# Kernel optimization log

Measured on AMD Instinct MI355X. Metric: run time of the kernel, lower is better.

Reference implementation:

```python
import jax, jax.numpy as jnp
import numpy as np

D_MODEL = 512
NUM_HEADS = 6
MIN_DIM = 8


def _compute_integer_dims(head_dims_float):
    # Faithful numpy port of torch _compute_integer_dims (runs under no_grad in torch,
    # so it is a constant w.r.t. autodiff; computed on concrete values here).
    hdf = np.asarray(head_dims_float)
    hdi = np.floor(hdf).astype(np.int64)
    diff = int(D_MODEL - hdi.sum())
    res = hdf - np.floor(hdf)
    if diff > 0:
        idx = np.argsort(-res)[:diff]  # topk largest residuals
        hdi[idx] += 1
    elif diff < 0:
        idx = np.argsort(res)[:(-diff)]  # topk of -residuals = smallest residuals
        hdi[idx] -= 1
    return hdi


def setup_inputs() -> dict:
    key = jax.random.key(0)
    k1, k2, k3, k4, k5, k6 = jax.random.split(key, 6)
    B, T = 4, 2048
    s = 1.0 / np.sqrt(D_MODEL).astype(np.float32)
    return {
        "query": jax.random.normal(k1, (B, T, D_MODEL), dtype=jnp.float32),
        "head_weight_logits": jax.random.normal(k2, (NUM_HEADS,), dtype=jnp.float32),
        "w_qkv": jax.random.normal(k3, (D_MODEL, 3 * D_MODEL), dtype=jnp.float32) * s,
        "b_qkv": jax.random.normal(k4, (3 * D_MODEL,), dtype=jnp.float32) * 0.01,
        "w_out": jax.random.normal(k5, (D_MODEL, D_MODEL), dtype=jnp.float32) * s,
        "b_out": jax.random.normal(k6, (D_MODEL,), dtype=jnp.float32) * 0.01,
    }


def reference(query, head_weight_logits, w_qkv, b_qkv, w_out, b_out):
    head_ratios = jax.nn.softmax(head_weight_logits, axis=0)
    head_dims_float = MIN_DIM + head_ratios * (D_MODEL - MIN_DIM * NUM_HEADS)
    hdi = _compute_integer_dims(jax.lax.stop_gradient(head_dims_float))  # concrete ints

    qkv = query @ w_qkv + b_qkv                      # [B,T,3*D]
    q_all, k_all, v_all = jnp.split(qkv, 3, axis=-1)  # each [B,T,D]

    outs = []
    start = 0
    for i in range(NUM_HEADS):  # small fixed loop; heads have distinct ragged widths
        dim = int(hdi[i])
        q = q_all[..., start:start + dim]
        k = k_all[..., start:start + dim]
        v = v_all[..., start:start + dim]
        start += dim
        scores = jnp.einsum('btd,bsd->bts', q, k) / (float(dim) ** 0.5)  # [B,T,T]
        attn = jax.nn.softmax(scores, axis=-1)
        outs.append(jnp.einsum('bts,bsd->btd', attn, v))

    output = jnp.concatenate(outs, axis=-1) @ w_out + b_out  # [B,T,D]

    hdi_f = jnp.asarray(hdi, dtype=head_dims_float.dtype)
    float_loss = (head_dims_float.sum() - D_MODEL) ** 2 \
        + jnp.mean(jax.nn.relu(MIN_DIM - head_dims_float))
    int_loss = jnp.mean((head_dims_float - hdi_f) ** 2)
    return output, float_loss + 0.5 * int_loss
```

## Files before the change

kernel.cpp:

```cpp
#include <hip/hip_runtime.h>
#include <hip/hip_bf16.h>
#include <cstdint>

typedef __attribute__((ext_vector_type(8))) __bf16 bf16x8;
typedef __attribute__((ext_vector_type(8))) unsigned short u16x8;
typedef __attribute__((ext_vector_type(4))) float f32x4;

#define QKSTRIDE 640
#define QKROW 1280
#define VTPAD 528

static __device__ __forceinline__ unsigned short f2bf(float f) {
  __hip_bfloat16 h = __float2bfloat16(f);
  return *reinterpret_cast<unsigned short*>(&h);
}
static __device__ __forceinline__ float bf2f(unsigned short u) {
  union { unsigned v; float f; } c; c.v = ((unsigned)u) << 16; return c.f;
}
static __device__ __forceinline__ unsigned pack2bf(float a, float b) {
  return (unsigned)f2bf(a) | ((unsigned)f2bf(b) << 16);
}

static __device__ __forceinline__ void gload_lds16(const void* g, void* lds) {
  __builtin_amdgcn_global_load_lds(
      (const __attribute__((address_space(1))) unsigned int*)g,
      (__attribute__((address_space(3))) unsigned int*)lds, 16, 0, 0);
}

__global__ void prep_kernel(const float* __restrict__ logits, int* __restrict__ hdr,
                            int* __restrict__ cmap, int* __restrict__ sched,
                            float* __restrict__ loss_out) {
  __shared__ int sh_starts[8], sh_astarts[8];
  __shared__ int sh_ax[24], sh_apos[24], sh_ah[24], sh_ab[24];
  const int tid = threadIdx.x;
  if (blockIdx.x != 0) return;

  if (tid == 0) {
    float l[6]; float mx = -1e30f;
    for (int i = 0; i < 6; ++i) { l[i] = logits[i]; mx = fmaxf(mx, l[i]); }
    float e[6]; float s = 0.f;
    for (int i = 0; i < 6; ++i) { e[i] = expf(l[i] - mx); s += e[i]; }
    float hdf[6]; float sumh = 0.f;
    for (int i = 0; i < 6; ++i) { hdf[i] = 8.0f + (e[i] / s) * 464.0f; sumh += hdf[i]; }
    int hdi[6]; float res[6]; int isum = 0;
    for (int i = 0; i < 6; ++i) {
      float fl = floorf(hdf[i]);
      hdi[i] = (int)fl; res[i] = hdf[i] - fl; isum += hdi[i];
    }
    int diff = 512 - isum;
    bool used[6] = {false, false, false, false, false, false};
    if (diff > 0) {
      for (int t = 0; t < diff; ++t) {
        int best = -1; float bv = -1e30f;
        for (int i = 0; i < 6; ++i) if (!used[i] && res[i] > bv) { bv = res[i]; best = i; }
        used[best] = true; hdi[best] += 1;
      }
    } else if (diff < 0) {
      for (int t = 0; t < -diff; ++t) {
        int best = -1; float bv = 1e30f;
        for (int i = 0; i < 6; ++i) if (!used[i] && res[i] < bv) { bv = res[i]; best = i; }
        used[best] = true; hdi[best] -= 1;
      }
    }
    { int st = 0, ast = 0;
      for (int i = 0; i < 6; ++i) {
        sh_starts[i] = st; sh_astarts[i] = ast;
        hdr[i] = hdi[i]; hdr[8 + i] = st; hdr[16 + i] = ast;
        st += hdi[i]; ast += (hdi[i] + 7) & ~7;
      }
      sh_starts[6] = st; sh_starts[7] = st;
    }
    int csth[6];
    for (int i = 0; i < 6; ++i) {
      int ncl = (hdi[i] + 31) / 32;
      int ntl = (hdi[i] + 15) / 16;
      csth[i] = 4 * ncl + 2 * ntl + 8;
    }
    int ord[6] = {0, 1, 2, 3, 4, 5};
    for (int a = 0; a < 6; ++a)
      for (int c = a + 1; c < 6; ++c)
        if (csth[ord[c]] > csth[ord[a]]) { int t = ord[a]; ord[a] = ord[c]; ord[c] = t; }
    int binload[8], bincnt[8];
    for (int x = 0; x < 8; ++x) { binload[x] = 0; bincnt[x] = 0; }
    int na = 0;
    for (int a = 0; a < 6; ++a) {
      const int hh = ord[a];
      for (int bb = 0; bb < 4; ++bb) {
        int best = -1;
        for (int x = 0; x < 8; ++x)
          if (bincnt[x] + 64 <= 192 && (best < 0 || binload[x] < binload[best])) best = x;
        if (best < 0) best = 0;
        sh_ax[na] = best; sh_apos[na] = bincnt[best];
        sh_ah[na] = hh; sh_ab[na] = bb; ++na;
        bincnt[best] += 64;
        binload[best] += csth[hh];
      }
    }
    float dv = sumh - 512.0f;
    float floss = dv * dv;
    float rsum = 0.f;
    for (int i = 0; i < 6; ++i) rsum += fmaxf(8.0f - hdf[i], 0.0f);
    floss += rsum / 6.0f;
    float il = 0.f;
    for (int i = 0; i < 6; ++i) { float dd = hdf[i] - (float)hdi[i]; il += dd * dd; }
    il /= 6.0f;
    loss_out[0] = floss + 0.5f * il;
  }
  __syncthreads();

  for (int col = tid; col < 512; col += 64) {
    int hh = 5;
    for (int i = 0; i < 5; ++i) if (col < sh_starts[i + 1]) { hh = i; break; }
    int qc = sh_astarts[hh] + (col - sh_starts[hh]);
    cmap[col] = qc;
    cmap[512 + col] = QKSTRIDE + qc;
    cmap[1024 + col] = 4096 + col;
    cmap[1536 + col] = hh;
  }
  for (int e = tid; e < 1536; e += 64) sched[e] = -1;
  __syncthreads();
  for (int e = tid; e < 24 * 64; e += 64) {
    const int a = e >> 6, qi = e & 63;
    sched[sh_ax[a] + 8 * (sh_apos[a] + qi)] = sh_ah[a] | (sh_ab[a] << 4) | (qi << 8);
  }
}

__global__ void conv_bf16_kernel(const float* __restrict__ x, unsigned short* __restrict__ y, int n4) {
  int i = blockIdx.x * blockDim.x + threadIdx.x;
  if (i >= n4) return;
  float4 v = reinterpret_cast<const float4*>(x)[i];
  union { unsigned short u[4]; uint2 q; } o;
  o.u[0] = f2bf(v.x); o.u[1] = f2bf(v.y); o.u[2] = f2bf(v.z); o.u[3] = f2bf(v.w);
  reinterpret_cast<uint2*>(y)[i] = o.q;
}

__global__ void convWT2_kernel(const float* __restrict__ Wqkv, const float* __restrict__ Wout,
                               unsigned short* __restrict__ wqkvT, unsigned short* __restrict__ woutT) {
  __shared__ float tile[64][65];
  const int mz = blockIdx.z;
  if (mz && blockIdx.y >= 8) return;
  const int N = mz ? 512 : 1536;
  const float* W = mz ? Wout : Wqkv;
  unsigned short* WT = mz ? woutT : wqkvT;
  const int k0 = blockIdx.x * 64, n0 = blockIdx.y * 64;
  const int t = threadIdx.x;
  {
    const int c = (t & 15) * 4;
#pragma unroll
    for (int rp = 0; rp < 4; ++rp) {
      const int r = rp * 16 + (t >> 4);
      float4 v = *reinterpret_cast<const float4*>(&W[(size_t)(k0 + r) * N + n0 + c]);
      tile[r][c] = v.x; tile[r][c + 1] = v.y; tile[r][c + 2] = v.z; tile[r][c + 3] = v.w;
    }
  }
  __syncthreads();
  {
    const int n = t >> 2, kc = (t & 3) * 16;
    unsigned short outv[16];
#pragma unroll
    for (int j = 0; j < 16; ++j) outv[j] = f2bf(tile[kc + j][n]);
    unsigned short* dst = &WT[(size_t)(n0 + n) * 512 + k0 + kc];
    *reinterpret_cast<u16x8*>(dst) = *reinterpret_cast<u16x8*>(&outv[0]);
    *reinterpret_cast<u16x8*>(dst + 8) = *reinterpret_cast<u16x8*>(&outv[8]);
  }
}

template<int MODE>
__global__ __launch_bounds__(256, 2) void gemm_bt(
    const unsigned short* __restrict__ A,
    const unsigned short* __restrict__ Bt,
    const float* __restrict__ bias,
    float* __restrict__ Cf,
    unsigned short* __restrict__ qkpad,
    unsigned short* __restrict__ VtOut,
    const int* __restrict__ cmap,
    int N, int K)
{
  __shared__ unsigned short As[128 * 32];
  __shared__ unsigned short Bs[128 * 32];
  const int tid = threadIdx.x;
  const int wave = tid >> 6, lane = tid & 63;
  const int lrow = lane & 15, lgrp = lane >> 4;
  const int wm = wave >> 1, wn = wave & 1;
  const int brow = blockIdx.y * 128;
  const int bcol = blockIdx.x * 128;

  f32x4 acc[4][4];
#pragma unroll
  for (int m = 0; m < 4; ++m)
#pragma unroll
    for (int n = 0; n < 4; ++n) acc[m][n] = (f32x4){0.f, 0.f, 0.f, 0.f};

  const int sig0 = wave * 128 + lane;
  for (int kb = 0; kb < K; kb += 32) {
    __syncthreads();
#pragma unroll
    for (int it = 0; it < 2; ++it) {
      const int sigma = sig0 + it * 64;
      const int r = sigma >> 2, sp = sigma & 3;
      const int sl = sp ^ ((r >> 1) & 3);
      gload_lds16(&A[(size_t)(brow + r) * K + kb + sl * 8], &As[sigma * 8]);
    }
#pragma unroll
    for (int it = 0; it < 2; ++it) {
      const int sigma = sig0 + it * 64;
      const int r = sigma >> 2, sp = sigma & 3;
      const int sl = sp ^ ((r >> 1) & 3);
      gload_lds16(&Bt[(size_t)(bcol + r) * K + kb + sl * 8], &Bs[sigma * 8]);
    }
    __syncthreads();
    const int sub = (lgrp ^ ((lrow >> 1) & 3)) * 8;
    bf16x8 aF[4], bF[4];
#pragma unroll
    for (int m = 0; m < 4; ++m)
      aF[m] = *reinterpret_cast<const bf16x8*>(&As[(wm * 64 + m * 16 + lrow) * 32 + sub]);
#pragma unroll
    for (int n = 0; n < 4; ++n)
      bF[n] = *reinterpret_cast<const bf16x8*>(&Bs[(wn * 64 + n * 16 + lrow) * 32 + sub]);
#pragma unroll
    for (int m = 0; m < 4; ++m)
#pragma unroll
      for (int n = 0; n < 4; ++n)
        acc[m][n] = __builtin_amdgcn_mfma_f32_16x16x32_bf16(aF[m], bF[n], acc[m][n], 0, 0, 0);
  }

#pragma unroll
  for (int n = 0; n < 4; ++n) {
    const int col = bcol + wn * 64 + n * 16 + lrow;
    const float bv = bias[col];
    int mc = 0;
    if (MODE == 1) mc = cmap[col];
#pragma unroll
    for (int m = 0; m < 4; ++m) {
      if (MODE == 0) {
#pragma unroll
        for (int r = 0; r < 4; ++r) {
          const int row = brow + wm * 64 + m * 16 + lgrp * 4 + r;
          Cf[(size_t)row * N + col] = acc[m][n][r] + bv;
        }
      } else if (mc < 4096) {
#pragma unroll
        for (int r = 0; r < 4; ++r) {
          const int row = brow + wm * 64 + m * 16 + lgrp * 4 + r;
          qkpad[(size_t)row * QKROW + mc] = f2bf(acc[m][n][r] + bv);
        }
      } else {
        const int t0g = brow + wm * 64 + m * 16 + lgrp * 4;
        const int b = t0g >> 11, t0 = t0g & 2047;
        uint2 w;
        w.x = pack2bf(acc[m][n][0] + bv, acc[m][n][1] + bv);
        w.y = pack2bf(acc[m][n][2] + bv, acc[m][n][3] + bv);
        *reinterpret_cast<uint2*>(&VtOut[(size_t)(b * VTPAD + (mc - 4096)) * 2048 + t0]) = w;
      }
    }
  }
}

template<int NC>
static __device__ __forceinline__ void attn_body(
    const unsigned short* __restrict__ qkpad,
    const unsigned short* __restrict__ Vt,
    unsigned short* __restrict__ Op,
    float2* __restrict__ mlArr,
    int b, int q0, int d, int start, int astart, int kh, int mlBase,
    unsigned char* KsB, unsigned int* PlW,
    int wave, int lane)
{
  constexpr int S = (4 * NC + 7) & ~7;
  constexpr int NT2 = 2 * NC;
  constexpr int KI = S / 8;
  constexpr int KTILE = 32 * S * 16;
  const int ntiles = (d + 15) >> 4;
  const int lrow = lane & 15, lgrp = lane >> 4;
  const float scale = 1.0f / sqrtf((float)d);

  bf16x8 qf[NC];
  {
    const unsigned short* qp = qkpad + (size_t)(b * 2048 + q0 + lrow) * QKROW + astart + lgrp * 8;
#pragma unroll
    for (int dc = 0; dc < NC; ++dc) {
      bf16x8 v = *reinterpret_cast<const bf16x8*>(qp + dc * 32);
#pragma unroll
      for (int j = 0; j < 8; ++j)
        if (dc * 32 + lgrp * 8 + j >= d) v[j] = (__bf16)0.0f;
      qf[dc] = v;
    }
  }

  const unsigned short* kPtr[KI];
  int kDstB[KI];
#pragma unroll
  for (int j = 0; j < KI; ++j) {
    const int g = (wave * KI + j) * 64 + lane;
    const int r = g / S, pp = g - r * S;
    const int sp = pp ^ (r & 7);
    kPtr[j] = qkpad + (size_t)(b * 2048 + kh * 1024 + r) * QKROW + QKSTRIDE + astart + sp * 8;
    kDstB[j] = g * 16;
  }

  const unsigned short* vRow = Vt + (size_t)(b * VTPAD + start + lrow) * 2048 + kh * 1024 + lgrp * 8;

  f32x4 acc[NT2];
#pragma unroll
  for (int t = 0; t < NT2; ++t) acc[t] = (f32x4){0.f, 0.f, 0.f, 0.f};
  float m_run = -1e30f, l_run = 0.f;

#pragma unroll
  for (int j = 0; j < KI; ++j) gload_lds16(kPtr[j], KsB + kDstB[j]);
#pragma unroll
  for (int j = 0; j < KI; ++j) kPtr[j] += 32 * QKROW;
  __syncthreads();

  for (int i = 0; i < 32; ++i) {
    const int kt = i << 5;
    const int cur = i & 1;
    if (i < 31) {
      unsigned char* kd = KsB + (cur ^ 1) * KTILE;
#pragma unroll
      for (int j = 0; j < KI; ++j) gload_lds16(kPtr[j], kd + kDstB[j]);
#pragma unroll
      for (int j = 0; j < KI; ++j) kPtr[j] += 32 * QKROW;
    }

    f32x4 s4[2];
    s4[0] = (f32x4){0.f, 0.f, 0.f, 0.f};
    s4[1] = (f32x4){0.f, 0.f, 0.f, 0.f};
    const unsigned char* kB = KsB + cur * KTILE;
    const int swz = lrow & 7;
    __builtin_amdgcn_s_setprio(1);
#pragma unroll
    for (int dc = 0; dc < NC; ++dc) {
#pragma unroll
      for (int t = 0; t < 2; ++t) {
        const bf16x8 kf = *reinterpret_cast<const bf16x8*>(
            kB + (t * 16 + lrow) * (S * 16) + (((dc * 4 + lgrp) ^ swz) * 16));
        s4[t] = __builtin_amdgcn_mfma_f32_16x16x32_bf16(kf, qf[dc], s4[t], 0, 0, 0);
      }
    }
    __builtin_amdgcn_s_setprio(0);

    float ps[8];
#pragma unroll
    for (int t = 0; t < 2; ++t)
#pragma unroll
      for (int r = 0; r < 4; ++r) ps[t * 4 + r] = s4[t][r] * scale;
    float pm = ps[0];
#pragma unroll
    for (int z = 1; z < 8; ++z) pm = fmaxf(pm, ps[z]);
    pm = fmaxf(pm, __shfl_xor(pm, 16));
    pm = fmaxf(pm, __shfl_xor(pm, 32));
    if (__any(pm > m_run + 8.0f)) {
      const float mn = fmaxf(m_run, pm);
      const float alpha = __expf(m_run - mn);
      m_run = mn; l_run *= alpha;
      float al4[4];
#pragma unroll
      for (int r = 0; r < 4; ++r) al4[r] = __shfl(alpha, lgrp * 4 + r);
#pragma unroll
      for (int t = 0; t < NT2; ++t) {
        if (t < ntiles) {
#pragma unroll
          for (int r = 0; r < 4; ++r) acc[t][r] *= al4[r];
        }
      }
    }
    float sum = 0.f;
#pragma unroll
    for (int z = 0; z < 8; ++z) { ps[z] = __expf(ps[z] - m_run); sum += ps[z]; }
    sum += __shfl_xor(sum, 16);
    sum += __shfl_xor(sum, 32);
    l_run += sum;

#pragma unroll
    for (int t = 0; t < 2; ++t) {
      uint2 w;
      w.x = pack2bf(ps[t * 4 + 0], ps[t * 4 + 1]);
      w.y = pack2bf(ps[t * 4 + 2], ps[t * 4 + 3]);
      *reinterpret_cast<uint2*>(PlW + lrow * 20 + 8 * t + 2 * lgrp) = w;
    }
    asm volatile("s_waitcnt lgkmcnt(0)" ::: "memory");
    __builtin_amdgcn_sched_barrier(0);
    const bf16x8 pa = *reinterpret_cast<const bf16x8*>(PlW + lrow * 20 + 4 * lgrp);

#pragma unroll
    for (int t0 = 0; t0 < NT2; t0 += 8) {
      bf16x8 vf[8];
#pragma unroll
      for (int j = 0; j < 8; ++j) {
        const int t = t0 + j;
        if (t < NT2 && t < ntiles)
          vf[j] = *reinterpret_cast<const bf16x8*>(vRow + (size_t)t * 32768 + kt);
      }
      __builtin_amdgcn_s_setprio(1);
#pragma unroll
      for (int j = 0; j < 8; ++j) {
        const int t = t0 + j;
        if (t < NT2 && t < ntiles)
          acc[t] = __builtin_amdgcn_mfma_f32_16x16x32_bf16(pa, vf[j], acc[t], 0, 0, 0);
      }
      __builtin_amdgcn_s_setprio(0);
    }
    __syncthreads();
  }

  float invl[4];
#pragma unroll
  for (int r = 0; r < 4; ++r) invl[r] = 1.0f / __shfl(l_run, lgrp * 4 + r);
#pragma unroll
  for (int t = 0; t < NT2; ++t) {
    if (t < ntiles) {
      const int col = t * 16 + lrow;
      if (col < d) {
#pragma unroll
        for (int r = 0; r < 4; ++r) {
          Op[(size_t)(b * 2048 + q0 + lgrp * 4 + r) * 512 + start + col] =
              f2bf(acc[t][r] * invl[r]);
        }
      }
    }
  }
  if (lgrp == 0) mlArr[mlBase + lrow] = make_float2(m_run, l_run);
}

__global__ __launch_bounds__(256, 3) void attn_fused(
    const unsigned short* __restrict__ qkpad,
    const unsigned short* __restrict__ Vt,
    unsigned short* __restrict__ O0,
    unsigned short* __restrict__ O1,
    float2* __restrict__ mlArr,
    const int* __restrict__ hdr,
    const int* __restrict__ sched)
{
  __shared__ __align__(16) unsigned char KsB[32768];
  __shared__ unsigned int Pl[4][16 * 20];

  const int sv = sched[blockIdx.x];
  if (sv < 0) return;
  const int h = sv & 15, b = (sv >> 4) & 15;
  const int qi = (sv >> 8) & 63;
  const int qb = qi & 31, kh = qi >> 5;
  const int d = hdr[h];
  const int nc = (d + 31) >> 5;
  if (nc > 8) return;
  const int start = hdr[8 + h];
  const int astart = hdr[16 + h];
  const int wave = threadIdx.x >> 6, lane = threadIdx.x & 63;
  const int q0 = qb * 64 + wave * 16;
  unsigned short* Op = kh ? O1 : O0;
  const int mlBase = (kh * 24 + h * 4 + b) * 2048 + q0;

  unsigned int* PlW = &Pl[wave][0];
  switch (nc) {
    case 1: attn_body<1>(qkpad, Vt, Op, mlArr, b, q0, d, start, astart, kh, mlBase, KsB, PlW, wave, lane); break;
    case 2: attn_body<2>(qkpad, Vt, Op, mlArr, b, q0, d, start, astart, kh, mlBase, KsB, PlW, wave, lane); break;
    case 3: attn_body<3>(qkpad, Vt, Op, mlArr, b, q0, d, start, astart, kh, mlBase, KsB, PlW, wave, lane); break;
    case 4: attn_body<4>(qkpad, Vt, Op, mlArr, b, q0, d, start, astart, kh, mlBase, KsB, PlW, wave, lane); break;
    case 5: attn_body<5>(qkpad, Vt, Op, mlArr, b, q0, d, start, astart, kh, mlBase, KsB, PlW, wave, lane); break;
    case 6: attn_body<6>(qkpad, Vt, Op, mlArr, b, q0, d, start, astart, kh, mlBase, KsB, PlW, wave, lane); break;
    case 7: attn_body<7>(qkpad, Vt, Op, mlArr, b, q0, d, start, astart, kh, mlBase, KsB, PlW, wave, lane); break;
    case 8: attn_body<8>(qkpad, Vt, Op, mlArr, b, q0, d, start, astart, kh, mlBase, KsB, PlW, wave, lane); break;
    default: break;
  }
}

__global__ __launch_bounds__(256) void merge_kernel(
    const unsigned short* __restrict__ O0,
    const unsigned short* __restrict__ O1,
    const float2* __restrict__ mlArr,
    unsigned short* __restrict__ attnC,
    const int* __restrict__ hdr)
{
  const int sh = blockIdx.y;
  const int h = sh >> 2, b = sh & 3;
  const int d = hdr[h];
  if (((d + 31) >> 5) > 8) return;
  const int start = hdr[8 + h];
  const int q = blockIdx.x * 32 + (threadIdx.x >> 3);
  const int cg = threadIdx.x & 7;
  const float2 A = mlArr[(h * 4 + b) * 2048 + q];
  const float2 B = mlArr[(24 + h * 4 + b) * 2048 + q];
  const float M = fmaxf(A.x, B.x);
  const float a1 = __expf(A.x - M) * A.y;
  const float a2 = __expf(B.x - M) * B.y;
  const float inv = 1.0f / (a1 + a2);
  const float r1 = a1 * inv, r2 = a2 * inv;
  const size_t base = (size_t)(b * 2048 + q) * 512 + start;
  for (int c = cg; c < d; c += 8)
    attnC[base + c] = f2bf(r1 * bf2f(O0[base + c]) + r2 * bf2f(O1[base + c]));
}

template<int NCLO, int NCHI>
__global__ __launch_bounds__(256, 2) void attn_kernel(
    const unsigned short* __restrict__ qkpad,
    const unsigned short* __restrict__ Vt,
    unsigned short* __restrict__ attnC,
    const int* __restrict__ hdr)
{
  const int h = blockIdx.y, b = blockIdx.z;
  const int d = hdr[h];
  const int nc = (d + 31) >> 5;
  if (nc <= NCLO || nc > NCHI) return;
  const int start = hdr[8 + h];
  const int astart = hdr[16 + h];
  const int wave = threadIdx.x >> 6;
  const int lane = threadIdx.x & 63;
  const int lrow = lane & 15, lgrp = lane >> 4;
  const int q0 = blockIdx.x * 64 + wave * 16;
  const int ntiles = (d + 15) >> 4;
  const float scale = 1.0f / sqrtf((float)d);

  __shared__ unsigned short Pl[2][4][16 * 32];

  bf16x8 qf[NCHI];
  {
    const size_t qbase = (size_t)(b * 2048 + q0 + lrow) * QKROW + astart;
#pragma unroll
    for (int dc = 0; dc < NCHI; ++dc) {
      if (dc < nc) {
        bf16x8 v = *reinterpret_cast<const bf16x8*>(&qkpad[qbase + dc * 32 + lgrp * 8]);
#pragma unroll
        for (int j = 0; j < 8; ++j)
          if (dc * 32 + lgrp * 8 + j >= d) v[j] = (__bf16)0.0f;
        qf[dc] = v;
      }
    }
  }

  f32x4 acc[2 * NCHI];
#pragma unroll
  for (int t = 0; t < 2 * NCHI; ++t) acc[t] = (f32x4){0.f, 0.f, 0.f, 0.f};
  float m_run[4] = {-1e30f, -1e30f, -1e30f, -1e30f};
  float l_run[4] = {0.f, 0.f, 0.f, 0.f};

  for (int kt = 0; kt < 2048; kt += 32) {
    f32x4 s0 = {0.f, 0.f, 0.f, 0.f}, s1 = {0.f, 0.f, 0.f, 0.f};
    const size_t kb0 = (size_t)(b * 2048 + kt + lrow) * QKROW + QKSTRIDE + astart;
    const size_t kb1 = kb0 + (size_t)16 * QKROW;
#pragma unroll
    for (int dc = 0; dc < NCHI; ++dc) {
      if (dc < nc) {
        bf16x8 k0 = *reinterpret_cast<const bf16x8*>(&qkpad[kb0 + dc * 32 + lgrp * 8]);
        bf16x8 k1 = *reinterpret_cast<const bf16x8*>(&qkpad[kb1 + dc * 32 + lgrp * 8]);
        s0 = __builtin_amdgcn_mfma_f32_16x16x32_bf16(qf[dc], k0, s0, 0, 0, 0);
        s1 = __builtin_amdgcn_mfma_f32_16x16x32_bf16(qf[dc], k1, s1, 0, 0, 0);
      }
    }
    float p0[4], p1[4], pmax[4];
#pragma unroll
    for (int r = 0; r < 4; ++r) {
      p0[r] = s0[r] * scale; p1[r] = s1[r] * scale;
      float mx = fmaxf(p0[r], p1[r]);
#pragma unroll
      for (int off = 1; off < 16; off <<= 1) mx = fmaxf(mx, __shfl_xor(mx, off));
      pmax[r] = mx;
    }
    bool need = false;
#pragma unroll
    for (int r = 0; r < 4; ++r) need = need || (pmax[r] > m_run[r] + 8.0f);
    if (__any(need)) {
#pragma unroll
      for (int r = 0; r < 4; ++r) {
        float mn = fmaxf(m_run[r], pmax[r]);
        float al = __expf(m_run[r] - mn);
        m_run[r] = mn; l_run[r] *= al;
#pragma unroll
        for (int t = 0; t < 2 * NCHI; ++t)
          if (t < ntiles) acc[t][r] *= al;
      }
    }
#pragma unroll
    for (int r = 0; r < 4; ++r) {
      p0[r] = __expf(p0[r] - m_run[r]);
      p1[r] = __expf(p1[r] - m_run[r]);
      float sm = p0[r] + p1[r];
#pragma unroll
      for (int off = 1; off < 16; off <<= 1) sm += __shfl_xor(sm, off);
      l_run[r] += sm;
    }
    const int pb = (kt >> 5) & 1;
    unsigned short* P = &Pl[pb][wave][0];
#pragma unroll
    for (int r = 0; r < 4; ++r) {
      P[(lgrp * 4 + r) * 32 + lrow] = f2bf(p0[r]);
      P[(lgrp * 4 + r) * 32 + 16 + lrow] = f2bf(p1[r]);
    }
    asm volatile("s_waitcnt lgkmcnt(0)" ::: "memory");
    bf16x8 pf = *reinterpret_cast<const bf16x8*>(&P[lrow * 32 + lgrp * 8]);
    const size_t vbase = (size_t)(b * VTPAD + start) * 2048 + kt + lgrp * 8;
#pragma unroll
    for (int t = 0; t < 2 * NCHI; ++t) {
      if (t < ntiles) {
        bf16x8 vf = *reinterpret_cast<const bf16x8*>(&Vt[vbase + (size_t)(t * 16 + lrow) * 2048]);
        acc[t] = __builtin_amdgcn_mfma_f32_16x16x32_bf16(pf, vf, acc[t], 0, 0, 0);
      }
    }
  }

  float inv[4];
#pragma unroll
  for (int r = 0; r < 4; ++r) inv[r] = 1.0f / l_run[r];
#pragma unroll
  for (int t = 0; t < 2 * NCHI; ++t) {
    if (t < ntiles) {
      int col = t * 16 + lrow;
      if (col < d) {
#pragma unroll
        for (int r = 0; r < 4; ++r) {
          attnC[(size_t)(b * 2048 + q0 + lgrp * 4 + r) * 512 + start + col] =
              f2bf(acc[t][r] * inv[r]);
        }
      }
    }
  }
}

extern "C" void kernel_launch(void* const* d_in, const int* in_sizes, int n_in,
                              void* d_out, int out_size, void* d_ws, size_t ws_size,
                              hipStream_t stream) {
  const float* query  = (const float*)d_in[0];
  const float* logits = (const float*)d_in[1];
  const float* w_qkv  = (const float*)d_in[2];
  const float* b_qkv  = (const float*)d_in[3];
  const float* w_out  = (const float*)d_in[4];
  const float* b_out  = (const float*)d_in[5];
  float* out = (float*)d_out;

  char* p = (char*)d_ws;
  size_t off = 0;
  auto alloc = [&](size_t bytes) {
    void* r = p + off; off += (bytes + 255) & ~(size_t)255; return r;
  };
  int* hdr              = (int*)alloc(1024);
  int* cmap             = (int*)alloc(2048 * 4);
  int* sched            = (int*)alloc(1536 * 4);
  unsigned short* qbf   = (unsigned short*)alloc((size_t)8192 * 512 * 2);
  unsigned short* wqkvT = (unsigned short*)alloc((size_t)1536 * 512 * 2);
  unsigned short* woutT = (unsigned short*)alloc((size_t)512 * 512 * 2);
  unsigned short* qkpad = (unsigned short*)alloc((size_t)8192 * QKROW * 2 + 4096);
  unsigned short* vbuf  = (unsigned short*)alloc((size_t)8192 * 512 * 2);
  unsigned short* Vt    = (unsigned short*)alloc((size_t)4 * VTPAD * 2048 * 2 + 4096);
  unsigned short* attnC = (unsigned short*)alloc((size_t)8192 * 512 * 2);
  float2* mlArr         = (float2*)alloc((size_t)2 * 24 * 2048 * 8);
  (void)ws_size; (void)in_sizes; (void)n_in; (void)out_size;

  prep_kernel<<<1, 64, 0, stream>>>(logits, hdr, cmap, sched, out + 4194304);
  conv_bf16_kernel<<<4096, 256, 0, stream>>>(query, qbf, 8192 * 512 / 4);
  convWT2_kernel<<<dim3(8, 24, 2), 256, 0, stream>>>(w_qkv, w_out, wqkvT, woutT);
  gemm_bt<1><<<dim3(12, 64), 256, 0, stream>>>(qbf, wqkvT, b_qkv, nullptr, qkpad, Vt, cmap, 1536, 512);
  attn_fused<<<dim3(1536, 1, 1), 256, 0, stream>>>(qkpad, Vt, qbf, vbuf, mlArr, hdr, sched);
  attn_kernel<8, 15><<<dim3(32, 6, 4), 256, 0, stream>>>(qkpad, Vt, attnC, hdr);
  merge_kernel<<<dim3(64, 24), 256, 0, stream>>>(qbf, vbuf, mlArr, attnC, hdr);
  gemm_bt<0><<<dim3(4, 64), 256, 0, stream>>>(attnC, woutT, b_out, out, nullptr, nullptr, nullptr, 512, 512);
}
```

Before: 284.2 us.

## Split wide-head attention blocks across output-dim halves and rebalance schedule

For heads with more than four 32-column chunks, each block now covers 32 queries instead of 64, and pairs of waves split the output head dimension in halves. Each wave holds at most 8 accumulator tiles, so register pressure drops and the launch bound goes from 3 to 4 blocks per CU. The scheduler assigns 128 slots to wide heads with a larger per-bin capacity, and the grid grows to 2560 blocks. The trade-off is that QK^T and softmax are computed twice, once per wave in each pair, which adds redundant compute and K loads.

```diff
diff --git a/kernel.cpp b/kernel.cpp
--- a/kernel.cpp
+++ b/kernel.cpp
@@ -31,7 +31,7 @@
                             int* __restrict__ cmap, int* __restrict__ sched,
                             float* __restrict__ loss_out) {
   __shared__ int sh_starts[8], sh_astarts[8];
-  __shared__ int sh_ax[24], sh_apos[24], sh_ah[24], sh_ab[24];
+  __shared__ int sh_ax[24], sh_apos[24], sh_ah[24], sh_ab[24], sh_nb[24];
   const int tid = threadIdx.x;
   if (blockIdx.x != 0) return;
 
@@ -70,11 +70,12 @@
       }
       sh_starts[6] = st; sh_starts[7] = st;
     }
-    int csth[6];
+    int csth[6], nbh6[6];
     for (int i = 0; i < 6; ++i) {
       int ncl = (hdi[i] + 31) / 32;
       int ntl = (hdi[i] + 15) / 16;
       csth[i] = 4 * ncl + 2 * ntl + 8;
+      nbh6[i] = (ncl <= 4) ? 64 : 128;
     }
     int ord[6] = {0, 1, 2, 3, 4, 5};
     for (int a = 0; a < 6; ++a)
@@ -85,14 +86,15 @@
     int na = 0;
     for (int a = 0; a < 6; ++a) {
       const int hh = ord[a];
+      const int nb = nbh6[hh];
       for (int bb = 0; bb < 4; ++bb) {
         int best = -1;
         for (int x = 0; x < 8; ++x)
-          if (bincnt[x] + 64 <= 192 && (best < 0 || binload[x] < binload[best])) best = x;
+          if (bincnt[x] + nb <= 320 && (best < 0 || binload[x] < binload[best])) best = x;
         if (best < 0) best = 0;
         sh_ax[na] = best; sh_apos[na] = bincnt[best];
-        sh_ah[na] = hh; sh_ab[na] = bb; ++na;
-        bincnt[best] += 64;
+        sh_ah[na] = hh; sh_ab[na] = bb; sh_nb[na] = nb; ++na;
+        bincnt[best] += nb;
         binload[best] += csth[hh];
       }
     }
@@ -117,11 +119,12 @@
     cmap[1024 + col] = 4096 + col;
     cmap[1536 + col] = hh;
   }
-  for (int e = tid; e < 1536; e += 64) sched[e] = -1;
+  for (int e = tid; e < 2560; e += 64) sched[e] = -1;
   __syncthreads();
-  for (int e = tid; e < 24 * 64; e += 64) {
-    const int a = e >> 6, qi = e & 63;
-    sched[sh_ax[a] + 8 * (sh_apos[a] + qi)] = sh_ah[a] | (sh_ab[a] << 4) | (qi << 8);
+  for (int e = tid; e < 24 * 128; e += 64) {
+    const int a = e >> 7, qi = e & 127;
+    if (qi < sh_nb[a])
+      sched[sh_ax[a] + 8 * (sh_apos[a] + qi)] = sh_ah[a] | (sh_ab[a] << 4) | (qi << 8);
   }
 }
 
@@ -256,21 +259,24 @@
   }
 }
 
-template<int NC>
+template<int NC, int NS>
 static __device__ __forceinline__ void attn_body(
     const unsigned short* __restrict__ qkpad,
     const unsigned short* __restrict__ Vt,
     unsigned short* __restrict__ Op,
     float2* __restrict__ mlArr,
-    int b, int q0, int d, int start, int astart, int kh, int mlBase,
+    int b, int q0, int d, int start, int astart, int kh, int mlBase, int dh,
     unsigned char* KsB, unsigned int* PlW,
     int wave, int lane)
 {
   constexpr int S = (4 * NC + 7) & ~7;
-  constexpr int NT2 = 2 * NC;
+  constexpr int NTW = (NS == 2) ? 8 : 2 * NC;
+  constexpr int BATCH = (NS == 2) ? 4 : 8;
   constexpr int KI = S / 8;
   constexpr int KTILE = 32 * S * 16;
-  const int ntiles = (d + 15) >> 4;
+  const int TT0 = dh * 8;
+  int ntw = ((d + 15) >> 4) - TT0;
+  if (ntw > NTW) ntw = NTW;
   const int lrow = lane & 15, lgrp = lane >> 4;
   const float scale = 1.0f / sqrtf((float)d);
 
@@ -298,11 +304,11 @@
     kDstB[j] = g * 16;
   }
 
-  const unsigned short* vRow = Vt + (size_t)(b * VTPAD + start + lrow) * 2048 + kh * 1024 + lgrp * 8;
-
-  f32x4 acc[NT2];
-#pragma unroll
-  for (int t = 0; t < NT2; ++t) acc[t] = (f32x4){0.f, 0.f, 0.f, 0.f};
+  const unsigned short* vRow = Vt + (size_t)(b * VTPAD + start + TT0 * 16 + lrow) * 2048 + kh * 1024 + lgrp * 8;
+
+  f32x4 acc[NTW];
+#pragma unroll
+  for (int t = 0; t < NTW; ++t) acc[t] = (f32x4){0.f, 0.f, 0.f, 0.f};
   float m_run = -1e30f, l_run = 0.f;
 
 #pragma unroll
@@ -357,8 +363,8 @@
 #pragma unroll
       for (int r = 0; r < 4; ++r) al4[r] = __shfl(alpha, lgrp * 4 + r);
 #pragma unroll
-      for (int t = 0; t < NT2; ++t) {
-        if (t < ntiles) {
+      for (int t = 0; t < NTW; ++t) {
+        if (t < ntw) {
 #pragma unroll
           for (int r = 0; r < 4; ++r) acc[t][r] *= al4[r];
         }
@@ -383,19 +389,19 @@
     const bf16x8 pa = *reinterpret_cast<const bf16x8*>(PlW + lrow * 20 + 4 * lgrp);
 
 #pragma unroll
-    for (int t0 = 0; t0 < NT2; t0 += 8) {
-      bf16x8 vf[8];
-#pragma unroll
-      for (int j = 0; j < 8; ++j) {
+    for (int t0 = 0; t0 < NTW; t0 += BATCH) {
+      bf16x8 vf[BATCH];
+#pragma unroll
+      for (int j = 0; j < BATCH; ++j) {
         const int t = t0 + j;
-        if (t < NT2 && t < ntiles)
+        if (t < NTW && t < ntw)
           vf[j] = *reinterpret_cast<const bf16x8*>(vRow + (size_t)t * 32768 + kt);
       }
       __builtin_amdgcn_s_setprio(1);
 #pragma unroll
-      for (int j = 0; j < 8; ++j) {
+      for (int j = 0; j < BATCH; ++j) {
         const int t = t0 + j;
-        if (t < NT2 && t < ntiles)
+        if (t < NTW && t < ntw)
           acc[t] = __builtin_amdgcn_mfma_f32_16x16x32_bf16(pa, vf[j], acc[t], 0, 0, 0);
       }
       __builtin_amdgcn_s_setprio(0);
@@ -407,9 +413,9 @@
 #pragma unroll
   for (int r = 0; r < 4; ++r) invl[r] = 1.0f / __shfl(l_run, lgrp * 4 + r);
 #pragma unroll
-  for (int t = 0; t < NT2; ++t) {
-    if (t < ntiles) {
-      const int col = t * 16 + lrow;
+  for (int t = 0; t < NTW; ++t) {
+    if (t < ntw) {
+      const int col = (TT0 + t) * 16 + lrow;
       if (col < d) {
 #pragma unroll
         for (int r = 0; r < 4; ++r) {
@@ -419,10 +425,10 @@
       }
     }
   }
-  if (lgrp == 0) mlArr[mlBase + lrow] = make_float2(m_run, l_run);
-}
-
-__global__ __launch_bounds__(256, 3) void attn_fused(
+  if (lgrp == 0 && (NS == 1 || dh == 0)) mlArr[mlBase + lrow] = make_float2(m_run, l_run);
+}
+
+__global__ __launch_bounds__(256, 4) void attn_fused(
     const unsigned short* __restrict__ qkpad,
     const unsigned short* __restrict__ Vt,
     unsigned short* __restrict__ O0,
@@ -437,29 +443,40 @@
   const int sv = sched[blockIdx.x];
   if (sv < 0) return;
   const int h = sv & 15, b = (sv >> 4) & 15;
-  const int qi = (sv >> 8) & 63;
-  const int qb = qi & 31, kh = qi >> 5;
+  const int qi = (sv >> 8) & 255;
   const int d = hdr[h];
   const int nc = (d + 31) >> 5;
   if (nc > 8) return;
   const int start = hdr[8 + h];
   const int astart = hdr[16 + h];
   const int wave = threadIdx.x >> 6, lane = threadIdx.x & 63;
-  const int q0 = qb * 64 + wave * 16;
-  unsigned short* Op = kh ? O1 : O0;
-  const int mlBase = (kh * 24 + h * 4 + b) * 2048 + q0;
-
   unsigned int* PlW = &Pl[wave][0];
-  switch (nc) {
-    case 1: attn_body<1>(qkpad, Vt, Op, mlArr, b, q0, d, start, astart, kh, mlBase, KsB, PlW, wave, lane); break;
-    case 2: attn_body<2>(qkpad, Vt, Op, mlArr, b, q0, d, start, astart, kh, mlBase, KsB, PlW, wave, lane); break;
-    case 3: attn_body<3>(qkpad, Vt, Op, mlArr, b, q0, d, start, astart, kh, mlBase, KsB, PlW, wave, lane); break;
-    case 4: attn_body<4>(qkpad, Vt, Op, mlArr, b, q0, d, start, astart, kh, mlBase, KsB, PlW, wave, lane); break;
-    case 5: attn_body<5>(qkpad, Vt, Op, mlArr, b, q0, d, start, astart, kh, mlBase, KsB, PlW, wave, lane); break;
-    case 6: attn_body<6>(qkpad, Vt, Op, mlArr, b, q0, d, start, astart, kh, mlBase, KsB, PlW, wave, lane); break;
-    case 7: attn_body<7>(qkpad, Vt, Op, mlArr, b, q0, d, start, astart, kh, mlBase, KsB, PlW, wave, lane); break;
-    case 8: attn_body<8>(qkpad, Vt, Op, mlArr, b, q0, d, start, astart, kh, mlBase, KsB, PlW, wave, lane); break;
-    default: break;
+
+  if (nc <= 4) {
+    const int kh = qi >> 5;
+    const int q0 = (qi & 31) * 64 + wave * 16;
+    unsigned short* Op = kh ? O1 : O0;
+    const int mlBase = (kh * 24 + h * 4 + b) * 2048 + q0;
+    switch (nc) {
+      case 1: attn_body<1, 1>(qkpad, Vt, Op, mlArr, b, q0, d, start, astart, kh, mlBase, 0, KsB, PlW, wave, lane); break;
+      case 2: attn_body<2, 1>(qkpad, Vt, Op, mlArr, b, q0, d, start, astart, kh, mlBase, 0, KsB, PlW, wave, lane); break;
+      case 3: attn_body<3, 1>(qkpad, Vt, Op, mlArr, b, q0, d, start, astart, kh, mlBase, 0, KsB, PlW, wave, lane); break;
+      case 4: attn_body<4, 1>(qkpad, Vt, Op, mlArr, b, q0, d, start, astart, kh, mlBase, 0, KsB, PlW, wave, lane); break;
+      default: break;
+    }
+  } else {
+    const int kh = qi >> 6;
+    const int q0 = (qi & 63) * 32 + (wave >> 1) * 16;
+    const int dh = wave & 1;
+    unsigned short* Op = kh ? O1 : O0;
+    const int mlBase = (kh * 24 + h * 4 + b) * 2048 + q0;
+    switch (nc) {
+      case 5: attn_body<5, 2>(qkpad, Vt, Op, mlArr, b, q0, d, start, astart, kh, mlBase, dh, KsB, PlW, wave, lane); break;
+      case 6: attn_body<6, 2>(qkpad, Vt, Op, mlArr, b, q0, d, start, astart, kh, mlBase, dh, KsB, PlW, wave, lane); break;
+      case 7: attn_body<7, 2>(qkpad, Vt, Op, mlArr, b, q0, d, start, astart, kh, mlBase, dh, KsB, PlW, wave, lane); break;
+      case 8: attn_body<8, 2>(qkpad, Vt, Op, mlArr, b, q0, d, start, astart, kh, mlBase, dh, KsB, PlW, wave, lane); break;
+      default: break;
+    }
   }
 }
 
@@ -632,7 +649,7 @@
   };
   int* hdr              = (int*)alloc(1024);
   int* cmap             = (int*)alloc(2048 * 4);
-  int* sched            = (int*)alloc(1536 * 4);
+  int* sched            = (int*)alloc(2560 * 4);
   unsigned short* qbf   = (unsigned short*)alloc((size_t)8192 * 512 * 2);
   unsigned short* wqkvT = (unsigned short*)alloc((size_t)1536 * 512 * 2);
   unsigned short* woutT = (unsigned short*)alloc((size_t)512 * 512 * 2);
@@ -647,7 +664,7 @@
   conv_bf16_kernel<<<4096, 256, 0, stream>>>(query, qbf, 8192 * 512 / 4);
   convWT2_kernel<<<dim3(8, 24, 2), 256, 0, stream>>>(w_qkv, w_out, wqkvT, woutT);
   gemm_bt<1><<<dim3(12, 64), 256, 0, stream>>>(qbf, wqkvT, b_qkv, nullptr, qkpad, Vt, cmap, 1536, 512);
-  attn_fused<<<dim3(1536, 1, 1), 256, 0, stream>>>(qkpad, Vt, qbf, vbuf, mlArr, hdr, sched);
+  attn_fused<<<dim3(2560, 1, 1), 256, 0, stream>>>(qkpad, Vt, qbf, vbuf, mlArr, hdr, sched);
   attn_kernel<8, 15><<<dim3(32, 6, 4), 256, 0, stream>>>(qkpad, Vt, attnC, hdr);
   merge_kernel<<<dim3(64, 24), 256, 0, stream>>>(qbf, vbuf, mlArr, attnC, hdr);
   gemm_bt<0><<<dim3(4, 64), 256, 0, stream>>>(attnC, woutT, b_out, out, nullptr, nullptr, nullptr, 512, 512);
```

Result: slower. 297.6 us (+4.7%).
